# Kernel tuning notes

Measured on AMD Instinct MI355X. Metric: run time of the kernel, lower is better.

Reference implementation:

```python
import jax, jax.numpy as jnp
import numpy as np

N_NODES = 50000
DROP_P = 0.25


def gcn_conv(x, edge_index, W, b, n_nodes):
    """PyG GCNConv: symmetric-normalized aggregation with self-loops.
    out = D^{-1/2} (A + I) D^{-1/2} (x @ W) + b
    """
    E = edge_index.shape[1]
    loops = jnp.arange(n_nodes, dtype=edge_index.dtype)
    src = jnp.concatenate([edge_index[0], loops])  # [E+N]
    dst = jnp.concatenate([edge_index[1], loops])  # [E+N]

    h = x @ W  # [N, out] dense GEMM

    ones = jnp.ones(E + n_nodes, dtype=x.dtype)
    deg = jax.ops.segment_sum(ones, dst, num_segments=n_nodes)  # [N]
    dinv = jnp.where(deg > 0, jax.lax.rsqrt(deg), 0.0)
    norm = dinv[src] * dinv[dst]  # [E+N]

    msgs = h[src] * norm[:, None]  # gather + scale, [E+N, out]
    out = jax.ops.segment_sum(msgs, dst, num_segments=n_nodes)  # scatter-add
    return out + b


def reference(x, edge_index, W1, b1, W2, b2):
    n = x.shape[0]
    h = gcn_conv(x, edge_index, W1, b1, n)
    h = jax.nn.elu(h)
    # F.dropout(p=0.25) defaults to training=True -> active dropout with
    # inverted scaling; deterministic mask from a fixed key.
    keep = jax.random.bernoulli(jax.random.key(42), 1.0 - DROP_P, h.shape)
    h = jnp.where(keep, h / (1.0 - DROP_P), 0.0).astype(h.dtype)
    out = gcn_conv(h, edge_index, W2, b2, n)
    return out


def setup_inputs() -> dict:
    key = jax.random.key(0)
    k1, k2, k3, k4 = jax.random.split(key, 4)
    C = 512
    E = 800000
    x = jax.random.normal(k1, (N_NODES, C), dtype=jnp.float32)
    edge_index = jax.random.randint(k2, (2, E), 0, N_NODES, dtype=jnp.int64)
    # Glorot-style scaled weights
    W1 = jax.random.normal(k3, (C, C // 2), dtype=jnp.float32) * (1.0 / np.sqrt(C))
    b1 = jnp.zeros((C // 2,), dtype=jnp.float32)
    W2 = jax.random.normal(k4, (C // 2, 1), dtype=jnp.float32) * (1.0 / np.sqrt(C // 2))
    b2 = jnp.zeros((1,), dtype=jnp.float32)
    return {"x": x, "edge_index": edge_index, "W1": W1, "b1": b1, "W2": W2, "b2": b2}
```

## Files before the change

kernel.cpp:

```cpp
#include <hip/hip_runtime.h>
#include <stdint.h>


typedef float floatx4 __attribute__((ext_vector_type(4)));
typedef _Float16 f16;
typedef _Float16 f16x8 __attribute__((ext_vector_type(8)));

union F16x8 {
  f16x8 v;
  f16 e[8];
  uint4 q;
};

__device__ __forceinline__ void tf_round(uint32_t& x0, uint32_t& x1, int r) {
  x0 += x1;
  x1 = (x1 << r) | (x1 >> (32 - r));
  x1 ^= x0;
}

__device__ __forceinline__ void threefry_0_42(uint32_t c0, uint32_t c1,
                                              uint32_t& o0, uint32_t& o1) {
  const uint32_t ks0 = 0u;
  const uint32_t ks1 = 42u;
  const uint32_t ks2 = 0x1BD11BDAu ^ 0u ^ 42u;
  uint32_t x0 = c0 + ks0;
  uint32_t x1 = c1 + ks1;
  tf_round(x0, x1, 13); tf_round(x0, x1, 15); tf_round(x0, x1, 26); tf_round(x0, x1, 6);
  x0 += ks1; x1 += ks2 + 1u;
  tf_round(x0, x1, 17); tf_round(x0, x1, 29); tf_round(x0, x1, 16); tf_round(x0, x1, 24);
  x0 += ks2; x1 += ks0 + 2u;
  tf_round(x0, x1, 13); tf_round(x0, x1, 15); tf_round(x0, x1, 26); tf_round(x0, x1, 6);
  x0 += ks0; x1 += ks1 + 3u;
  tf_round(x0, x1, 17); tf_round(x0, x1, 29); tf_round(x0, x1, 16); tf_round(x0, x1, 24);
  x0 += ks1; x1 += ks2 + 4u;
  tf_round(x0, x1, 13); tf_round(x0, x1, 15); tf_round(x0, x1, 26); tf_round(x0, x1, 6);
  x0 += ks2; x1 += ks0 + 5u;
  o0 = x0; o1 = x1;
}

__device__ __forceinline__ unsigned char mask_byte(uint32_t b) {
  uint32_t jb = b << 3;
  uint32_t m = 0;
#pragma unroll
  for (int i = 0; i < 8; ++i) {
    uint32_t r0, r1;
    threefry_0_42(0u, jb + (uint32_t)i, r0, r1);
    uint32_t bits = r0 ^ r1;
    m |= (bits < 0xC0000000u ? 1u : 0u) << i;
  }
  return (unsigned char)m;
}

__global__ void k_deg(const int* __restrict__ dst, int E, int* __restrict__ deg,
                      unsigned char* __restrict__ maskb, int nb0) {
  int t = blockIdx.x * blockDim.x + threadIdx.x;
  if (t < E) atomicAdd(&deg[dst[t]], 1);
  if (t < nb0) maskb[t] = mask_byte((uint32_t)t);
}

__global__ __launch_bounds__(256) void k_scan1(const int* __restrict__ deg,
                                               int* __restrict__ excl,
                                               int* __restrict__ sums,
                                               float* __restrict__ dinv, int N) {
  __shared__ int sm[256];
  int tid = threadIdx.x;
  int i = blockIdx.x * 256 + tid;
  int v = (i < N) ? deg[i] : 0;
  if (i < N) dinv[i] = 1.0f / sqrtf((float)(v + 1));
  sm[tid] = v;
  __syncthreads();
#pragma unroll
  for (int off = 1; off < 256; off <<= 1) {
    int t = (tid >= off) ? sm[tid - off] : 0;
    __syncthreads();
    sm[tid] += t;
    __syncthreads();
  }
  if (i < N) excl[i] = sm[tid] - v;
  if (tid == 255) sums[blockIdx.x] = sm[255];
}

__global__ __launch_bounds__(1024) void k_scan2(int* __restrict__ sums, int nb) {
  __shared__ int sm[1024];
  int tid = threadIdx.x;
  int v = (tid < nb) ? sums[tid] : 0;
  sm[tid] = v;
  __syncthreads();
#pragma unroll
  for (int off = 1; off < 1024; off <<= 1) {
    int t = (tid >= off) ? sm[tid - off] : 0;
    __syncthreads();
    sm[tid] += t;
    __syncthreads();
  }
  if (tid < nb) sums[tid] = sm[tid] - v;
}

__global__ void k_scan3(int* __restrict__ rowptr, int* __restrict__ cursor,
                        const int* __restrict__ sums, int N, int E) {
  int i = blockIdx.x * blockDim.x + threadIdx.x;
  if (i < N) {
    int r = rowptr[i] + sums[i >> 8];
    rowptr[i] = r;
    cursor[i] = r;
  }
  if (i == 0) rowptr[N] = E;
}

__global__ void k_bucket(const int* __restrict__ src, const int* __restrict__ dst,
                         int* __restrict__ cursor, int* __restrict__ csr_src, int E,
                         unsigned char* __restrict__ maskb, int nb0, int nb1) {
  int t = blockIdx.x * blockDim.x + threadIdx.x;
  if (t < E) {
    int pos = atomicAdd(&cursor[dst[t]], 1);
    csr_src[pos] = src[t];
  }
  if (t < nb1) maskb[nb0 + t] = mask_byte((uint32_t)(nb0 + t));
}

__global__ void k_prep_w1t(const float* __restrict__ W1,
                           f16* __restrict__ Bpk) {
  int t = blockIdx.x * blockDim.x + threadIdx.x;
  if (t >= 512 * 256) return;
  int k = t >> 8, n = t & 255;
  int ks = k >> 5, quad = (k >> 3) & 3, j = k & 7;
  int nt = n >> 4, lane = quad * 16 + (n & 15);
  size_t e = ((size_t)(ks * 16 + nt)) * 64 + lane;
  Bpk[e * 8 + j] = (f16)W1[t];
}

__global__ __launch_bounds__(256) void k_gemm_mfma(
    const float* __restrict__ A,
    const uint4* __restrict__ Bpk,
    const float* __restrict__ dinv,
    f16* __restrict__ C,
    int M) {
  __shared__ char As[64 * 1024];
  const int tid = threadIdx.x;
  const int cg = tid >> 6;
  const int lane = tid & 63;
  const int quad = lane >> 4;
  const int l16 = lane & 15;
  const int m0 = blockIdx.x * 64;

  auto cvt8 = [](float4 a, float4 b) {
    F16x8 r;
    r.e[0] = (f16)a.x; r.e[1] = (f16)a.y; r.e[2] = (f16)a.z; r.e[3] = (f16)a.w;
    r.e[4] = (f16)b.x; r.e[5] = (f16)b.y; r.e[6] = (f16)b.z; r.e[7] = (f16)b.w;
    return r;
  };

  {
    const int srow = tid >> 2;
    const int scq = tid & 3;
    int grow = m0 + srow;
    if (grow >= M) grow = M - 1;
    const float* gsp = A + (size_t)grow * 512 + scq * 8;
    char* lbase = As + srow * 1024;
    const int swz = (srow & 7) << 4;
#pragma unroll
    for (int ks = 0; ks < 16; ++ks) {
      float4 s0 = *(const float4*)(gsp + ks * 32);
      float4 s1 = *(const float4*)(gsp + ks * 32 + 4);
      *(uint4*)(lbase + ((scq * 16 + ks * 64) ^ swz)) = cvt8(s0, s1).q;
    }
  }
  __syncthreads();

  floatx4 acc[4][4];
#pragma unroll
  for (int fr = 0; fr < 4; ++fr)
#pragma unroll
    for (int t = 0; t < 4; ++t) acc[fr][t] = (floatx4){0.f, 0.f, 0.f, 0.f};

  const uint4* bp0 = Bpk + lane + (size_t)(cg * 4) * 64;
  const int swzr = (l16 & 7) << 4;

#pragma unroll
  for (int ks = 0; ks < 16; ++ks) {
    const uint4* bp = bp0 + (size_t)ks * 1024;
    F16x8 bf[4];
#pragma unroll
    for (int t = 0; t < 4; ++t) bf[t].q = bp[t * 64];

#pragma unroll
    for (int fr = 0; fr < 4; ++fr) {
      const int row = fr * 16 + l16;
      F16x8 af;
      af.q = *(const uint4*)(As + row * 1024 + ((quad * 16 + ks * 64) ^ swzr));
#pragma unroll
      for (int t = 0; t < 4; ++t) {
        acc[fr][t] = __builtin_amdgcn_mfma_f32_16x16x32_f16(af.v, bf[t].v, acc[fr][t], 0, 0, 0);
      }
    }
  }

#pragma unroll
  for (int fr = 0; fr < 4; ++fr)
#pragma unroll
    for (int r = 0; r < 4; ++r) {
      int gm = m0 + fr * 16 + quad * 4 + r;
      if (gm < M) {
        float dv = dinv[gm];
#pragma unroll
        for (int t = 0; t < 4; ++t) {
          const int col = (cg * 4 + t) * 16 + l16;
          C[(size_t)gm * 256 + col] = (f16)(dv * acc[fr][t][r]);
        }
      }
    }
}

__global__ __launch_bounds__(256) void k_gather_fused(
    const int* __restrict__ rowptr, const int* __restrict__ csr_src,
    const float* __restrict__ dinv, const f16* __restrict__ hs,
    const float* __restrict__ b1, const float* __restrict__ W2,
    const unsigned char* __restrict__ maskb,
    float* __restrict__ zs, int N) {
  int wave = (blockIdx.x * blockDim.x + threadIdx.x) >> 6;
  int lane = threadIdx.x & 63;
  int half = lane >> 5;
  int l = lane & 31;
  int d = wave * 2 + half;
  bool valid = d < N;
  if (!valid) d = N - 1;
  float dd = dinv[d];
  int beg = rowptr[d], end = rowptr[d + 1];
  int f0 = l << 3;

  F16x8 accu;
  accu.q = *(const uint4*)(hs + ((size_t)d << 8) + f0);
  f16x8 accv = accu.v;

  int e = beg;
  {
    int pe = beg + ((4 - (beg & 3)) & 3);
    if (pe > end) pe = end;
    for (; e < pe; ++e) {
      F16x8 a;
      a.q = *(const uint4*)(hs + ((size_t)csr_src[e] << 8) + f0);
      accv = accv + a.v;
    }
  }
  for (; e + 3 < end; e += 4) {
    int4 s4 = *(const int4*)(csr_src + e);
    F16x8 a, b, c, dq;
    a.q  = *(const uint4*)(hs + ((size_t)s4.x << 8) + f0);
    b.q  = *(const uint4*)(hs + ((size_t)s4.y << 8) + f0);
    c.q  = *(const uint4*)(hs + ((size_t)s4.z << 8) + f0);
    dq.q = *(const uint4*)(hs + ((size_t)s4.w << 8) + f0);
    f16x8 t0 = a.v + b.v;
    f16x8 t1 = c.v + dq.v;
    accv = accv + (t0 + t1);
  }
  for (; e < end; ++e) {
    F16x8 a;
    a.q = *(const uint4*)(hs + ((size_t)csr_src[e] << 8) + f0);
    accv = accv + a.v;
  }
  accu.v = accv;

  float4 bb0 = *(const float4*)(b1 + f0);
  float4 bb1 = *(const float4*)(b1 + f0 + 4);
  float4 w0  = *(const float4*)(W2 + f0);
  float4 w1  = *(const float4*)(W2 + f0 + 4);
  const float* bbp[8] = {&bb0.x, &bb0.y, &bb0.z, &bb0.w, &bb1.x, &bb1.y, &bb1.z, &bb1.w};
  const float* wp[8]  = {&w0.x, &w0.y, &w0.z, &w0.w, &w1.x, &w1.y, &w1.z, &w1.w};

  uint32_t mb = maskb[(size_t)d * 32 + l];

  float sum = 0.f;
#pragma unroll
  for (int i = 0; i < 8; ++i) {
    float va = dd * (float)accu.e[i] + *bbp[i];
    float ea = va > 0.f ? va : (__expf(va) - 1.0f);
    float ha = ((mb >> i) & 1u) ? (ea * (1.0f / 0.75f)) : 0.f;
    sum += ha * *wp[i];
  }
#pragma unroll
  for (int off = 16; off > 0; off >>= 1) sum += __shfl_down(sum, off, 32);
  if (l == 0 && valid) zs[d] = dd * sum;
}

__global__ __launch_bounds__(256) void k_gather2(
    const int* __restrict__ rowptr, const int* __restrict__ csr_src,
    const float* __restrict__ dinv, const float* __restrict__ zs,
    const float* __restrict__ b2, float* __restrict__ out, int N) {
  int wave = (blockIdx.x * blockDim.x + threadIdx.x) >> 6;
  int lane = threadIdx.x & 63;
  int sub = lane >> 4;
  int l = lane & 15;
  int d = wave * 4 + sub;
  bool valid = d < N;
  if (!valid) d = N - 1;
  float dd = dinv[d];
  int beg = rowptr[d], end = rowptr[d + 1];

  float acc = 0.f;
  for (int e = beg + l; e < end; e += 16) {
    acc += zs[csr_src[e]];
  }
#pragma unroll
  for (int off = 8; off > 0; off >>= 1) acc += __shfl_down(acc, off, 16);
  if (l == 0 && valid) out[d] = b2[0] + dd * (zs[d] + acc);
}

extern "C" void kernel_launch(void* const* d_in, const int* in_sizes, int n_in,
                              void* d_out, int out_size, void* d_ws, size_t ws_size,
                              hipStream_t stream) {
  const float* x  = (const float*)d_in[0];
  const int*   ei = (const int*)d_in[1];
  const float* W1 = (const float*)d_in[2];
  const float* b1 = (const float*)d_in[3];
  const float* W2 = (const float*)d_in[4];
  const float* b2 = (const float*)d_in[5];
  float* out = (float*)d_out;

  const int E = in_sizes[1] / 2;
  const int N = in_sizes[0] / 512;
  const int* src = ei;
  const int* dst = ei + E;

  char* ws = (char*)d_ws;
  size_t off = 0;
  auto alloc = [&](size_t bytes) -> void* {
    void* p = ws + off;
    off += (bytes + 255) & ~(size_t)255;
    return p;
  };
  int*   deg     = (int*)  alloc((size_t)N * 4);
  int*   rowptr  = (int*)  alloc((size_t)(N + 1) * 4);
  int*   cursor  = (int*)  alloc((size_t)N * 4);
  int*   csr_src = (int*)  alloc((size_t)E * 4);
  int*   sums    = (int*)  alloc(1024 * 4);
  float* dinv    = (float*)alloc((size_t)N * 4);
  f16*   hs      = (f16*)  alloc((size_t)N * 256 * 2);
  float* zs      = (float*)alloc((size_t)N * 4);
  f16*   Bpk     = (f16*)  alloc(512 * 256 * 2);
  unsigned char* maskb = (unsigned char*)alloc((size_t)N * 32);

  const int nb = (N + 255) / 256;

  const int nbytes = N * 32;
  const int nb0 = nbytes >> 1;
  const int nb1 = nbytes - nb0;
  const int tdeg = (E > nb0) ? E : nb0;
  const int tbkt = (E > nb1) ? E : nb1;

  hipMemsetAsync(deg, 0, (size_t)N * 4, stream);
  k_prep_w1t<<<(512 * 256 + 255) / 256, 256, 0, stream>>>(W1, Bpk);
  k_deg<<<(tdeg + 255) / 256, 256, 0, stream>>>(dst, E, deg, maskb, nb0);
  k_scan1<<<nb, 256, 0, stream>>>(deg, rowptr, sums, dinv, N);
  k_scan2<<<1, 1024, 0, stream>>>(sums, nb);
  k_scan3<<<(N + 255) / 256, 256, 0, stream>>>(rowptr, cursor, sums, N, E);
  k_bucket<<<(tbkt + 255) / 256, 256, 0, stream>>>(src, dst, cursor, csr_src, E,
                                                   maskb, nb0, nb1);

  k_gemm_mfma<<<(N + 63) / 64, 256, 0, stream>>>(x, (const uint4*)Bpk, dinv, hs, N);

  const int nwaves1 = (N + 1) / 2;
  k_gather_fused<<<(nwaves1 * 64 + 255) / 256, 256, 0, stream>>>(rowptr, csr_src, dinv, hs,
                                                                 b1, W2, maskb, zs, N);
  const int nwaves2 = (N + 3) / 4;
  k_gather2<<<(nwaves2 * 64 + 255) / 256, 256, 0, stream>>>(rowptr, csr_src, dinv, zs, b2, out, N);
}
```

Before: 338.2 us.

## Fuse CSR build, degree, scan and mask generation into one persistent kernel

Result: slower. 521.2 us (+54.1%).

```diff
diff --git a/kernel.cpp b/kernel.cpp
--- a/kernel.cpp
+++ b/kernel.cpp
@@ -11,6 +11,27 @@
   f16 e[8];
   uint4 q;
 };
+
+#define NB_BUILD 256
+#define NT_BUILD 1024
+
+__device__ __forceinline__ void gsync(int* bar) {
+  __syncthreads();
+  if (threadIdx.x == 0) {
+    __threadfence();
+    int g = __hip_atomic_load(&bar[1], __ATOMIC_RELAXED, __HIP_MEMORY_SCOPE_AGENT);
+    int a = __hip_atomic_fetch_add(&bar[0], 1, __ATOMIC_ACQ_REL, __HIP_MEMORY_SCOPE_AGENT);
+    if (a == (int)gridDim.x - 1) {
+      __hip_atomic_store(&bar[0], 0, __ATOMIC_RELAXED, __HIP_MEMORY_SCOPE_AGENT);
+      __hip_atomic_fetch_add(&bar[1], 1, __ATOMIC_RELEASE, __HIP_MEMORY_SCOPE_AGENT);
+    } else {
+      while (__hip_atomic_load(&bar[1], __ATOMIC_ACQUIRE, __HIP_MEMORY_SCOPE_AGENT) == g)
+        __builtin_amdgcn_s_sleep(2);
+    }
+    __threadfence();
+  }
+  __syncthreads();
+}
 
 __device__ __forceinline__ void tf_round(uint32_t& x0, uint32_t& x1, int r) {
   x0 += x1;
@@ -51,82 +72,85 @@
   return (unsigned char)m;
 }
 
-__global__ void k_deg(const int* __restrict__ dst, int E, int* __restrict__ deg,
-                      unsigned char* __restrict__ maskb, int nb0) {
-  int t = blockIdx.x * blockDim.x + threadIdx.x;
-  if (t < E) atomicAdd(&deg[dst[t]], 1);
-  if (t < nb0) maskb[t] = mask_byte((uint32_t)t);
-}
-
-__global__ __launch_bounds__(256) void k_scan1(const int* __restrict__ deg,
-                                               int* __restrict__ excl,
-                                               int* __restrict__ sums,
-                                               float* __restrict__ dinv, int N) {
+__global__ __launch_bounds__(NT_BUILD, 4) void k_build(
+    const int* __restrict__ src, const int* __restrict__ dst, int E, int N,
+    const float* __restrict__ W1, f16* __restrict__ Bpk,
+    int* __restrict__ deg, int* __restrict__ rowptr, int* __restrict__ cursor,
+    int* __restrict__ csr_src, int* __restrict__ sums, float* __restrict__ dinv,
+    unsigned char* __restrict__ maskb, int nbytes, int* __restrict__ bar) {
+  const int tid = threadIdx.x;
+  const int gtid = blockIdx.x * NT_BUILD + tid;
+  const int gsz = NB_BUILD * NT_BUILD;
+
+  for (int i = gtid; i < N; i += gsz) deg[i] = 0;
+  for (int t = gtid; t < 512 * 256; t += gsz) {
+    int k = t >> 8, n = t & 255;
+    int ks = k >> 5, quad = (k >> 3) & 3, j = k & 7;
+    int nt2 = n >> 4, lane = quad * 16 + (n & 15);
+    Bpk[(((size_t)(ks * 16 + nt2)) * 64 + lane) * 8 + j] = (f16)W1[t];
+  }
+  for (int t = gtid; t < nbytes; t += gsz) maskb[t] = mask_byte((uint32_t)t);
+  gsync(bar);
+
+  for (int e = gtid; e < E; e += gsz) atomicAdd(&deg[dst[e]], 1);
+  gsync(bar);
+
+  const int CH = (N + NB_BUILD - 1) / NB_BUILD;
   __shared__ int sm[256];
-  int tid = threadIdx.x;
-  int i = blockIdx.x * 256 + tid;
-  int v = (i < N) ? deg[i] : 0;
-  if (i < N) dinv[i] = 1.0f / sqrtf((float)(v + 1));
-  sm[tid] = v;
+  const int base = blockIdx.x * CH;
+  const int idx = base + tid;
+  int v = 0;
+  if (tid < 256) {
+    v = (tid < CH && idx < N) ? deg[idx] : 0;
+    sm[tid] = v;
+  }
   __syncthreads();
 #pragma unroll
   for (int off = 1; off < 256; off <<= 1) {
-    int t = (tid >= off) ? sm[tid - off] : 0;
+    int t = 0;
+    if (tid < 256 && tid >= off) t = sm[tid - off];
     __syncthreads();
-    sm[tid] += t;
+    if (tid < 256) sm[tid] += t;
     __syncthreads();
   }
-  if (i < N) excl[i] = sm[tid] - v;
-  if (tid == 255) sums[blockIdx.x] = sm[255];
-}
-
-__global__ __launch_bounds__(1024) void k_scan2(int* __restrict__ sums, int nb) {
-  __shared__ int sm[1024];
-  int tid = threadIdx.x;
-  int v = (tid < nb) ? sums[tid] : 0;
-  sm[tid] = v;
-  __syncthreads();
-#pragma unroll
-  for (int off = 1; off < 1024; off <<= 1) {
-    int t = (tid >= off) ? sm[tid - off] : 0;
+  if (tid < 256 && tid < CH && idx < N) {
+    rowptr[idx] = sm[tid] - v;
+    dinv[idx] = 1.0f / sqrtf((float)(v + 1));
+  }
+  if (tid == 0) sums[blockIdx.x] = sm[CH - 1];
+  gsync(bar);
+
+  if (blockIdx.x == 0) {
+    int s2 = 0;
+    if (tid < 256) {
+      s2 = sums[tid];
+      sm[tid] = s2;
+    }
     __syncthreads();
-    sm[tid] += t;
-    __syncthreads();
-  }
-  if (tid < nb) sums[tid] = sm[tid] - v;
-}
-
-__global__ void k_scan3(int* __restrict__ rowptr, int* __restrict__ cursor,
-                        const int* __restrict__ sums, int N, int E) {
-  int i = blockIdx.x * blockDim.x + threadIdx.x;
-  if (i < N) {
-    int r = rowptr[i] + sums[i >> 8];
-    rowptr[i] = r;
-    cursor[i] = r;
-  }
-  if (i == 0) rowptr[N] = E;
-}
-
-__global__ void k_bucket(const int* __restrict__ src, const int* __restrict__ dst,
-                         int* __restrict__ cursor, int* __restrict__ csr_src, int E,
-                         unsigned char* __restrict__ maskb, int nb0, int nb1) {
-  int t = blockIdx.x * blockDim.x + threadIdx.x;
-  if (t < E) {
-    int pos = atomicAdd(&cursor[dst[t]], 1);
-    csr_src[pos] = src[t];
-  }
-  if (t < nb1) maskb[nb0 + t] = mask_byte((uint32_t)(nb0 + t));
-}
-
-__global__ void k_prep_w1t(const float* __restrict__ W1,
-                           f16* __restrict__ Bpk) {
-  int t = blockIdx.x * blockDim.x + threadIdx.x;
-  if (t >= 512 * 256) return;
-  int k = t >> 8, n = t & 255;
-  int ks = k >> 5, quad = (k >> 3) & 3, j = k & 7;
-  int nt = n >> 4, lane = quad * 16 + (n & 15);
-  size_t e = ((size_t)(ks * 16 + nt)) * 64 + lane;
-  Bpk[e * 8 + j] = (f16)W1[t];
+#pragma unroll
+    for (int off = 1; off < 256; off <<= 1) {
+      int t = 0;
+      if (tid < 256 && tid >= off) t = sm[tid - off];
+      __syncthreads();
+      if (tid < 256) sm[tid] += t;
+      __syncthreads();
+    }
+    if (tid < 256) sums[tid] = sm[tid] - s2;
+  }
+  gsync(bar);
+
+  if (tid < 256 && tid < CH && idx < N) {
+    int r = rowptr[idx] + sums[blockIdx.x];
+    rowptr[idx] = r;
+    cursor[idx] = r;
+  }
+  if (gtid == 0) rowptr[N] = E;
+  gsync(bar);
+
+  for (int e = gtid; e < E; e += gsz) {
+    int pos = atomicAdd(&cursor[dst[e]], 1);
+    csr_src[pos] = src[e];
+  }
 }
 
 __global__ __launch_bounds__(256) void k_gemm_mfma(
@@ -338,23 +362,14 @@
   float* zs      = (float*)alloc((size_t)N * 4);
   f16*   Bpk     = (f16*)  alloc(512 * 256 * 2);
   unsigned char* maskb = (unsigned char*)alloc((size_t)N * 32);
-
-  const int nb = (N + 255) / 256;
+  int*   bar     = (int*)  alloc(256);
 
   const int nbytes = N * 32;
-  const int nb0 = nbytes >> 1;
-  const int nb1 = nbytes - nb0;
-  const int tdeg = (E > nb0) ? E : nb0;
-  const int tbkt = (E > nb1) ? E : nb1;
-
-  hipMemsetAsync(deg, 0, (size_t)N * 4, stream);
-  k_prep_w1t<<<(512 * 256 + 255) / 256, 256, 0, stream>>>(W1, Bpk);
-  k_deg<<<(tdeg + 255) / 256, 256, 0, stream>>>(dst, E, deg, maskb, nb0);
-  k_scan1<<<nb, 256, 0, stream>>>(deg, rowptr, sums, dinv, N);
-  k_scan2<<<1, 1024, 0, stream>>>(sums, nb);
-  k_scan3<<<(N + 255) / 256, 256, 0, stream>>>(rowptr, cursor, sums, N, E);
-  k_bucket<<<(tbkt + 255) / 256, 256, 0, stream>>>(src, dst, cursor, csr_src, E,
-                                                   maskb, nb0, nb1);
+
+  hipMemsetAsync(bar, 0, 8, stream);
+  k_build<<<NB_BUILD, NT_BUILD, 0, stream>>>(src, dst, E, N, W1, Bpk, deg, rowptr,
+                                             cursor, csr_src, sums, dinv, maskb,
+                                             nbytes, bar);
 
   k_gemm_mfma<<<(N + 63) / 64, 256, 0, stream>>>(x, (const uint4*)Bpk, dinv, hs, N);
 
```
